# Performance work log

Measured on AMD Instinct MI355X. Metric: run time of the kernel, lower is better.

Reference implementation:

```python
import jax, jax.numpy as jnp
import numpy as np

# Straight-through-estimator round (round_pass in the original code)
def _round_ste(x):
    return x + jax.lax.stop_gradient(jnp.round(x) - x)

INPUT_QMAX = 127.0   # 2**(input_bit-1)-1,  input_bit=8
WEIGHT_QMAX = 127.0  # 2**(weight_bit-1)-1, weight_bit=8
OUT_RANGE = 127.0    # 2**(output_bit-1)-1, output_bit=8


def setup_inputs() -> dict:
    key = jax.random.key(0)
    k0, k1, k2 = jax.random.split(key, 3)
    B, Cin, Cout, H, W, K = 16, 320, 320, 64, 64, 3
    x = jax.random.normal(k0, (B, Cin, H, W), dtype=jnp.float32)
    weight = jax.random.normal(k1, (Cout, Cin, K, K), dtype=jnp.float32) * 0.05
    bias = jax.random.normal(k2, (Cout,), dtype=jnp.float32) * 0.1
    # LSQ learned scalar step sizes (cloned from conv_lsq in the original)
    step_x = jnp.float32(0.02)
    step_w = jnp.float32(0.002)
    step_b = jnp.float32(0.01)
    # Bit_shift_layer scale: shift conv accumulator down into output_bit range
    shift_scale = jnp.float32(2.0 ** -7)
    return {"x": x, "weight": weight, "bias": bias, "step_x": step_x,
            "step_w": step_w, "step_b": step_b, "shift_scale": shift_scale}


def reference(x, weight, bias, step_x, step_w, step_b, shift_scale):
    # --- lsq_quant_input (isint=True): x_int in [-127,127], x_scale = 1/step ---
    x_int = jnp.clip(_round_ste(x / step_x), -INPUT_QMAX, INPUT_QMAX)
    x_scale = 1.0 / step_x
    # --- lsq_quant_weight (isint=True) ---
    w_int = jnp.clip(_round_ste(weight / step_w), -WEIGHT_QMAX, WEIGHT_QMAX)
    w_scale = 1.0 / step_w
    # --- Conv2d_int: integer-valued conv (no bias) ---
    y_int = jax.lax.conv_general_dilated(
        x_int, w_int, window_strides=(1, 1), padding=((1, 1), (1, 1)),
        dimension_numbers=("NCHW", "OIHW", "NCHW"))
    # --- mvm_result_shift: bit-shift accumulator into output range ---
    y_shift = jnp.clip(_round_ste(y_int * shift_scale), -OUT_RANGE, OUT_RANGE)
    # --- lsq_quant_bias (isint=False): dequantized bias ---
    b_deq = jnp.clip(_round_ste(bias / step_b), -OUT_RANGE, OUT_RANGE) * step_b
    # --- bias requant to output int scale, add, clamp (fused epilogue) ---
    b_int8 = jnp.clip(_round_ste(b_deq * shift_scale * x_scale * w_scale),
                      -OUT_RANGE, OUT_RANGE)
    y_shift_dmac = jnp.clip(y_shift + b_int8[None, :, None, None],
                            -OUT_RANGE, OUT_RANGE)
    # module returns y_shift_DMAC (the integer-valued clamped output)
    return y_shift_dmac
```

## Files before the change

### kernel.cpp

```cpp
#include <hip/hip_runtime.h>

typedef int v4i __attribute__((ext_vector_type(4)));

#define QMAX 127.0f

#define XQ_BYTES 22302720
#define WQ_BYTES 921600

__device__ __forceinline__ float clampf(float v, float lo, float hi) {
    return fminf(fmaxf(v, lo), hi);
}

__device__ __forceinline__ float qround(float v, float step, float inv) {
    float t = v * inv;
    float r = rintf(t);
    float d = fabsf(t - r);
    if (fabsf(d - 0.5f) < fabsf(t) * 1e-5f + 1e-5f)
        r = rintf(v / step);
    return r;
}

__device__ __forceinline__ void gload_lds16(const char* g, char* l) {
    __builtin_amdgcn_global_load_lds(
        (const __attribute__((address_space(1))) void*)g,
        (__attribute__((address_space(3))) void*)l, 16, 0, 0);
}

__device__ __forceinline__ v4i mfma_i8(v4i a, v4i b, v4i c) {
    return __builtin_amdgcn_mfma_i32_16x16x64_i8(a, b, c, 0, 0, 0);
}

__global__ __launch_bounds__(256) void fused_prep_kernel(
    const float* __restrict__ x, const float* __restrict__ w,
    const float* __restrict__ bias,
    const float* __restrict__ step_x_p, const float* __restrict__ step_w_p,
    const float* __restrict__ step_b_p, const float* __restrict__ shift_p,
    char* __restrict__ xq, char* __restrict__ wq2, float* __restrict__ bi)
{
    __shared__ float F[16 * 577];
    const int bid = blockIdx.x;
    const int t = threadIdx.x;

    if (bid < 1024) {
        const int h = bid & 63;
        const int b = bid >> 6;
        const float step = *step_x_p;
        const float inv  = 1.0f / step;
        const int wcol = t >> 2;
        const int cg   = t & 3;
        v4i vals[5];

        for (int c5 = 0; c5 < 5; ++c5) {
            {
                const int r = t >> 4, c = (t & 15) * 4;
                const float* src = x + (((size_t)(b * 320 + c5 * 64) * 64 + h) * 64);
#pragma unroll
                for (int i = 0; i < 4; ++i) {
                    const int row = r + i * 16;
                    *(float4*)&F[row * 65 + c] =
                        *(const float4*)(src + (size_t)row * 4096 + c);
                }
            }
            __syncthreads();
            int dws[4];
#pragma unroll
            for (int j = 0; j < 4; ++j) {
                int word = 0;
#pragma unroll
                for (int k = 0; k < 4; ++k) {
                    float v = F[(cg * 16 + j * 4 + k) * 65 + wcol];
                    int xi = (int)clampf(qround(v, step, inv), -QMAX, QMAX);
                    word |= (xi & 0xFF) << (8 * k);
                }
                dws[j] = word;
            }
            vals[c5] = (v4i){dws[0], dws[1], dws[2], dws[3]};
            __syncthreads();
        }

        const int col = wcol + 1;
        const int key = (col >> 1) & 3;
        char* base = xq + ((size_t)(b * 66 + (h + 1)) * 66 + col) * 320;
#pragma unroll
        for (int c5 = 0; c5 < 5; ++c5)
            *(v4i*)(base + c5 * 64 + (((cg ^ key)) << 4)) = vals[c5];

    } else if (bid < 1124) {
        const int blk = bid - 1024;
        const int cog = blk / 5;
        const int c5  = blk - cog * 5;
        const int co0 = cog * 16;
        const float step = *step_w_p;
        const float inv  = 1.0f / step;

        for (int idx = t; idx < 2304; idx += 256) {
            const int co_l = idx / 144;
            const int m4   = idx - co_l * 144;
            const float4 v = *(const float4*)(
                w + (size_t)(co0 + co_l) * 2880 + c5 * 576 + m4 * 4);
            float* dst = &F[co_l * 577 + m4 * 4];
            dst[0] = v.x; dst[1] = v.y; dst[2] = v.z; dst[3] = v.w;
        }
        __syncthreads();

        const int co_l = (t >> 2) & 15;
        const int cib  = (t >> 6) * 16 + (t & 3) * 4;
        char* dst = wq2 + (size_t)(c5 * 20 + cog) * 1024 + t * 4;
#pragma unroll
        for (int p = 0; p < 9; ++p) {
            int word = 0;
#pragma unroll
            for (int k = 0; k < 4; ++k) {
                float v = F[co_l * 577 + (cib + k) * 9 + p];
                int q = (int)clampf(qround(v, step, inv), -QMAX, QMAX);
                word |= (q & 0xFF) << (8 * k);
            }
            *(int*)(dst + (size_t)p * 102400) = word;
        }
    } else if (bid < 1449) {
        int tid = (bid - 1124) * 256 + t;
        if (tid < 83200) {
            int b = tid / 5200;
            int r = tid - b * 5200;
            int px = r / 20;
            int ck = (r - px * 20) * 16;
            int row, col;
            if (px < 66)       { row = 0;  col = px; }
            else if (px < 132) { row = 65; col = px - 66; }
            else { int e = px - 132; row = 1 + (e >> 1); col = (e & 1) * 65; }
            size_t off = ((size_t)(b * 66 + row) * 66 + col) * 320 + ck;
            v4i z = {0, 0, 0, 0};
            *(v4i*)&xq[off] = z;
        }
    } else {
        const float step_b = *step_b_p;
        const float xs = 1.0f / *step_x_p;
        const float ws = 1.0f / *step_w_p;
        const float shift = *shift_p;
#pragma unroll
        for (int co = t; co < 320; co += 256) {
            float b_deq = clampf(rintf(bias[co] / step_b), -QMAX, QMAX) * step_b;
            float v = ((b_deq * shift) * xs) * ws;
            bi[co] = clampf(rintf(v), -QMAX, QMAX);
        }
    }
}

__global__ __launch_bounds__(256, 3) void conv_mfma_kernel(
    const char* __restrict__ xq, const char* __restrict__ wq2,
    const float* __restrict__ bi, const float* __restrict__ shift_p,
    float* __restrict__ out)
{
    __shared__ __attribute__((aligned(16))) char B_lds[2][25344];

    const int t  = threadIdx.x;
    const int id = blockIdx.x;
    const int g  = id / 40;
    const int r  = id - g * 40;
    const int bx = r >> 3;
    const int ptile = (g << 3) | (r & 7);

    const int co0 = bx * 64;
    const int b  = ptile >> 4;
    const int h0 = (ptile & 15) * 4;

    const int wave = t >> 6, lane = t & 63;
    const int quad = lane >> 4, l15 = lane & 15;

    const char* xbase = xq + ((size_t)(b * 66 + h0) * 66) * 320;

    v4i acc[4][4] = {};

    for (int c = t; c < 1584; c += 256) {
        const char* gp = xbase + (c >> 2) * 320 + ((c & 3) << 4);
        gload_lds16(gp, &B_lds[0][(c - lane) * 16]);
    }
    __syncthreads();

    for (int c5 = 0; c5 < 5; ++c5) {
        if (c5 < 4) {
            const int ci0 = (c5 + 1) * 64;
            char* dst = B_lds[(c5 + 1) & 1];
            for (int c = t; c < 1584; c += 256) {
                const char* gp = xbase + (c >> 2) * 320 + ci0 + ((c & 3) << 4);
                gload_lds16(gp, &dst[(c - lane) * 16]);
            }
        }

        const char* Bc = B_lds[c5 & 1];
        const char* wp = wq2 + (c5 * 20 + bx * 4) * 1024 + lane * 16;

        v4i areg[2][4];
#pragma unroll
        for (int cs = 0; cs < 4; ++cs)
            areg[0][cs] = *(const v4i*)(wp + 0 * 102400 + cs * 1024);

#pragma unroll
        for (int p = 0; p < 9; ++p) {
            const int dh = p / 3, dw = p - dh * 3;
            if (p < 8) {
#pragma unroll
                for (int cs = 0; cs < 4; ++cs)
                    areg[(p + 1) & 1][cs] =
                        *(const v4i*)(wp + (p + 1) * 102400 + cs * 1024);
            }
            const int prow = wave + dh;
            auto bread = [&](int i) -> v4i {
                const int col = i * 16 + l15 + dw;
                const int key = (col >> 1) & 3;
                return *(const v4i*)&Bc[(prow * 66 + col) * 64 +
                                        ((quad ^ key) << 4)];
            };
            v4i bf = bread(0);
#pragma unroll
            for (int i = 0; i < 4; ++i) {
                v4i bcur = bf;
                if (i < 3) bf = bread(i + 1);
                __builtin_amdgcn_s_setprio(1);
#pragma unroll
                for (int cs = 0; cs < 4; ++cs)
                    acc[cs][i] = mfma_i8(areg[p & 1][cs], bcur, acc[cs][i]);
                __builtin_amdgcn_s_setprio(0);
            }
        }
        __syncthreads();
    }

    const float shift = *shift_p;
    const int h = h0 + wave;
#pragma unroll
    for (int cs = 0; cs < 4; ++cs) {
#pragma unroll
        for (int reg = 0; reg < 4; ++reg) {
            const int co = co0 + cs * 16 + quad * 4 + reg;
            const float bv = bi[co];
            float* orow = out + (((size_t)(b * 320 + co) * 64) + h) * 64;
#pragma unroll
            for (int i = 0; i < 4; ++i) {
                float y  = (float)acc[cs][i][reg];
                float ys = clampf(rintf(y * shift), -QMAX, QMAX);
                orow[i * 16 + l15] = clampf(ys + bv, -QMAX, QMAX);
            }
        }
    }
}

extern "C" void kernel_launch(void* const* d_in, const int* in_sizes, int n_in,
                              void* d_out, int out_size, void* d_ws, size_t ws_size,
                              hipStream_t stream) {
    const float* x      = (const float*)d_in[0];
    const float* w      = (const float*)d_in[1];
    const float* bias   = (const float*)d_in[2];
    const float* step_x = (const float*)d_in[3];
    const float* step_w = (const float*)d_in[4];
    const float* step_b = (const float*)d_in[5];
    const float* shift  = (const float*)d_in[6];
    float* out = (float*)d_out;

    char*  xq  = (char*)d_ws;
    char*  wq2 = xq + XQ_BYTES;
    float* bi  = (float*)(wq2 + WQ_BYTES);

    fused_prep_kernel<<<1450, 256, 0, stream>>>(x, w, bias, step_x, step_w,
                                                step_b, shift, xq, wq2, bi);
    conv_mfma_kernel<<<1280, 256, 0, stream>>>(xq, wq2, bi, shift, out);
}
```

Measured before the change: 211.5 us.

## Switch conv MFMA from 16x16x64 to 32x32x32 int8 tiles with repacked weights

New measurement: 222.8 us. 5.3% more time.

```diff
diff --git a/kernel.cpp b/kernel.cpp
--- a/kernel.cpp
+++ b/kernel.cpp
@@ -1,6 +1,7 @@
 #include <hip/hip_runtime.h>
 
-typedef int v4i __attribute__((ext_vector_type(4)));
+typedef int v4i  __attribute__((ext_vector_type(4)));
+typedef int v16i __attribute__((ext_vector_type(16)));
 
 #define QMAX 127.0f
 
@@ -26,8 +27,8 @@
         (__attribute__((address_space(3))) void*)l, 16, 0, 0);
 }
 
-__device__ __forceinline__ v4i mfma_i8(v4i a, v4i b, v4i c) {
-    return __builtin_amdgcn_mfma_i32_16x16x64_i8(a, b, c, 0, 0, 0);
+__device__ __forceinline__ v16i mfma32_i8(v4i a, v4i b, v16i c) {
+    return __builtin_amdgcn_mfma_i32_32x32x32_i8(a, b, c, 0, 0, 0);
 }
 
 __global__ __launch_bounds__(256) void fused_prep_kernel(
@@ -37,7 +38,7 @@
     const float* __restrict__ step_b_p, const float* __restrict__ shift_p,
     char* __restrict__ xq, char* __restrict__ wq2, float* __restrict__ bi)
 {
-    __shared__ float F[16 * 577];
+    __shared__ float F[32 * 289];
     const int bid = blockIdx.x;
     const int t = threadIdx.x;
 
@@ -87,31 +88,32 @@
 
     } else if (bid < 1124) {
         const int blk = bid - 1024;
-        const int cog = blk / 5;
-        const int c5  = blk - cog * 5;
-        const int co0 = cog * 16;
+        const int cot = blk / 10;
+        const int rem = blk - cot * 10;
+        const int c5  = rem >> 1;
+        const int ks  = rem & 1;
         const float step = *step_w_p;
         const float inv  = 1.0f / step;
 
         for (int idx = t; idx < 2304; idx += 256) {
-            const int co_l = idx / 144;
-            const int m4   = idx - co_l * 144;
+            const int co_l = idx / 72;
+            const int m4   = idx - co_l * 72;
             const float4 v = *(const float4*)(
-                w + (size_t)(co0 + co_l) * 2880 + c5 * 576 + m4 * 4);
-            float* dst = &F[co_l * 577 + m4 * 4];
+                w + (size_t)(cot * 32 + co_l) * 2880 + c5 * 576 + ks * 288 + m4 * 4);
+            float* dst = &F[co_l * 289 + m4 * 4];
             dst[0] = v.x; dst[1] = v.y; dst[2] = v.z; dst[3] = v.w;
         }
         __syncthreads();
 
-        const int co_l = (t >> 2) & 15;
-        const int cib  = (t >> 6) * 16 + (t & 3) * 4;
-        char* dst = wq2 + (size_t)(c5 * 20 + cog) * 1024 + t * 4;
+        const int co_l = (t >> 2) & 31;
+        const int cib  = (t >> 7) * 16 + (t & 3) * 4;
+        char* dst = wq2 + (size_t)(c5 * 20 + ks * 10 + cot) * 1024 + t * 4;
 #pragma unroll
         for (int p = 0; p < 9; ++p) {
             int word = 0;
 #pragma unroll
             for (int k = 0; k < 4; ++k) {
-                float v = F[co_l * 577 + (cib + k) * 9 + p];
+                float v = F[co_l * 289 + (cib + k) * 9 + p];
                 int q = (int)clampf(qround(v, step, inv), -QMAX, QMAX);
                 word |= (q & 0xFF) << (8 * k);
             }
@@ -165,11 +167,11 @@
     const int h0 = (ptile & 15) * 4;
 
     const int wave = t >> 6, lane = t & 63;
-    const int quad = lane >> 4, l15 = lane & 15;
+    const int l31 = lane & 31, hi = lane >> 5;
 
     const char* xbase = xq + ((size_t)(b * 66 + h0) * 66) * 320;
 
-    v4i acc[4][4] = {};
+    v16i acc[2][2] = {};
 
     for (int c = t; c < 1584; c += 256) {
         const char* gp = xbase + (c >> 2) * 320 + ((c & 3) << 4);
@@ -188,40 +190,48 @@
         }
 
         const char* Bc = B_lds[c5 & 1];
-        const char* wp = wq2 + (c5 * 20 + bx * 4) * 1024 + lane * 16;
-
-        v4i areg[2][4];
-#pragma unroll
-        for (int cs = 0; cs < 4; ++cs)
-            areg[0][cs] = *(const v4i*)(wp + 0 * 102400 + cs * 1024);
+        const char* wp = wq2 + (c5 * 20 + bx * 2) * 1024 + lane * 16;
+
+        v4i areg[2][2][2];
+#pragma unroll
+        for (int ct = 0; ct < 2; ++ct)
+#pragma unroll
+            for (int ks = 0; ks < 2; ++ks)
+                areg[0][ct][ks] = *(const v4i*)(wp + ks * 10240 + ct * 1024);
 
 #pragma unroll
         for (int p = 0; p < 9; ++p) {
             const int dh = p / 3, dw = p - dh * 3;
             if (p < 8) {
 #pragma unroll
-                for (int cs = 0; cs < 4; ++cs)
-                    areg[(p + 1) & 1][cs] =
-                        *(const v4i*)(wp + (p + 1) * 102400 + cs * 1024);
+                for (int ct = 0; ct < 2; ++ct)
+#pragma unroll
+                    for (int ks = 0; ks < 2; ++ks)
+                        areg[(p + 1) & 1][ct][ks] = *(const v4i*)(
+                            wp + (p + 1) * 102400 + ks * 10240 + ct * 1024);
             }
             const int prow = wave + dh;
-            auto bread = [&](int i) -> v4i {
-                const int col = i * 16 + l15 + dw;
+            v4i bf[2][2];
+#pragma unroll
+            for (int h = 0; h < 2; ++h) {
+                const int col = h * 32 + l31 + dw;
                 const int key = (col >> 1) & 3;
-                return *(const v4i*)&Bc[(prow * 66 + col) * 64 +
-                                        ((quad ^ key) << 4)];
-            };
-            v4i bf = bread(0);
-#pragma unroll
-            for (int i = 0; i < 4; ++i) {
-                v4i bcur = bf;
-                if (i < 3) bf = bread(i + 1);
-                __builtin_amdgcn_s_setprio(1);
-#pragma unroll
-                for (int cs = 0; cs < 4; ++cs)
-                    acc[cs][i] = mfma_i8(areg[p & 1][cs], bcur, acc[cs][i]);
-                __builtin_amdgcn_s_setprio(0);
-            }
+                const int base = (prow * 66 + col) * 64;
+#pragma unroll
+                for (int ks = 0; ks < 2; ++ks)
+                    bf[h][ks] = *(const v4i*)&Bc[base +
+                                                 (((2 * ks + hi) ^ key) << 4)];
+            }
+            __builtin_amdgcn_s_setprio(1);
+#pragma unroll
+            for (int ks = 0; ks < 2; ++ks)
+#pragma unroll
+                for (int h = 0; h < 2; ++h)
+#pragma unroll
+                    for (int ct = 0; ct < 2; ++ct)
+                        acc[ct][h] = mfma32_i8(areg[p & 1][ct][ks], bf[h][ks],
+                                               acc[ct][h]);
+            __builtin_amdgcn_s_setprio(0);
         }
         __syncthreads();
     }
@@ -229,17 +239,18 @@
     const float shift = *shift_p;
     const int h = h0 + wave;
 #pragma unroll
-    for (int cs = 0; cs < 4; ++cs) {
-#pragma unroll
-        for (int reg = 0; reg < 4; ++reg) {
-            const int co = co0 + cs * 16 + quad * 4 + reg;
+    for (int ct = 0; ct < 2; ++ct) {
+#pragma unroll
+        for (int reg = 0; reg < 16; ++reg) {
+            const int row = (reg & 3) + 8 * (reg >> 2) + 4 * hi;
+            const int co = co0 + ct * 32 + row;
             const float bv = bi[co];
             float* orow = out + (((size_t)(b * 320 + co) * 64) + h) * 64;
 #pragma unroll
-            for (int i = 0; i < 4; ++i) {
-                float y  = (float)acc[cs][i][reg];
+            for (int hh = 0; hh < 2; ++hh) {
+                float y  = (float)acc[ct][hh][reg];
                 float ys = clampf(rintf(y * shift), -QMAX, QMAX);
-                orow[i * 16 + l15] = clampf(ys + bv, -QMAX, QMAX);
+                orow[hh * 32 + l31] = clampf(ys + bv, -QMAX, QMAX);
             }
         }
     }
```
